# Kernel tuning notes

Hardware: AMD Instinct MI355X
Metric: run time of the kernel (lower is better)

## Reference

```python
import jax, jax.numpy as jnp
import numpy as np

EMBED = 512
HEADS = 8
SCALE = 4
B, N = 2, 2048
DH = EMBED // HEADS
EPS = 1e-5


def _mha(q_in, k_in, v_in, wq, bq, wk, bk, wv, bv, wo, bo, causal):
    Bq, Nq, _ = q_in.shape
    Nk = k_in.shape[1]
    Q = (q_in @ wq + bq).reshape(Bq, Nq, HEADS, DH)
    K = (k_in @ wk + bk).reshape(Bq, Nk, HEADS, DH)
    V = (v_in @ wv + bv).reshape(Bq, Nk, HEADS, DH)
    # scores: [B, H, Nq, Nk]
    scores = jnp.einsum('bqhd,bkhd->bhqk', Q, K) / np.sqrt(DH).astype(np.float32)
    if causal:
        mask = jnp.triu(jnp.full((Nq, Nq), -jnp.inf, dtype=scores.dtype), k=1)
        scores = scores + mask[None, None]
    attn = jax.nn.softmax(scores, axis=-1)
    out = jnp.einsum('bhqk,bkhd->bqhd', attn, V).reshape(Bq, Nq, EMBED)
    return out @ wo + bo


def _ln(x, g, b):
    mu = jnp.mean(x, axis=-1, keepdims=True)
    var = jnp.var(x, axis=-1, keepdims=True)
    return (x - mu) * jax.lax.rsqrt(var + EPS) * g + b


def setup_inputs() -> dict:
    key = jax.random.key(0)
    ks = iter(jax.random.split(key, 32))
    p = lambda *s: 0.02 * jax.random.normal(next(ks), s, dtype=jnp.float32)
    inp = {
        'x': jax.random.normal(next(ks), (B, N, EMBED), dtype=jnp.float32),
        'encoder_output': jax.random.normal(next(ks), (B, N, EMBED), dtype=jnp.float32),
    }
    for pre in ('sa', 'ca'):
        inp[pre + '_wq'] = p(EMBED, EMBED); inp[pre + '_bq'] = jnp.zeros(EMBED)
        inp[pre + '_wk'] = p(EMBED, EMBED); inp[pre + '_bk'] = jnp.zeros(EMBED)
        inp[pre + '_wv'] = p(EMBED, EMBED); inp[pre + '_bv'] = jnp.zeros(EMBED)
        inp[pre + '_wo'] = p(EMBED, EMBED); inp[pre + '_bo'] = jnp.zeros(EMBED)
    for i in (1, 2, 3):
        inp[f'ln{i}_g'] = jnp.ones(EMBED); inp[f'ln{i}_b'] = jnp.zeros(EMBED)
    inp['ff_w1'] = p(EMBED, SCALE * EMBED); inp['ff_b1'] = jnp.zeros(SCALE * EMBED)
    inp['ff_w2'] = p(SCALE * EMBED, EMBED); inp['ff_b2'] = jnp.zeros(EMBED)
    return inp


def reference(x, encoder_output,
              sa_wq, sa_bq, sa_wk, sa_bk, sa_wv, sa_bv, sa_wo, sa_bo,
              ca_wq, ca_bq, ca_wk, ca_bk, ca_wv, ca_bv, ca_wo, ca_bo,
              ln1_g, ln1_b, ln2_g, ln2_b, ln3_g, ln3_b,
              ff_w1, ff_b1, ff_w2, ff_b2):
    x = _mha(x, x, x, sa_wq, sa_bq, sa_wk, sa_bk, sa_wv, sa_bv, sa_wo, sa_bo, True) + x
    x = _ln(x, ln1_g, ln1_b)
    x = _mha(x, encoder_output, encoder_output,
             ca_wq, ca_bq, ca_wk, ca_bk, ca_wv, ca_bv, ca_wo, ca_bo, False) + x
    x = _ln(x, ln2_g, ln2_b)
    h = jax.nn.gelu(x @ ff_w1 + ff_b1, approximate=False)
    x = h @ ff_w2 + ff_b2 + x
    return _ln(x, ln3_g, ln3_b)
```

## Files before the change

kernel.cpp:

```cpp
#include <hip/hip_runtime.h>
#include <hip/hip_bf16.h>

typedef __bf16 bf16x8 __attribute__((ext_vector_type(8)));
typedef float f32x4 __attribute__((ext_vector_type(4)));
typedef unsigned short u16;

#define EMB 512
#define FF 2048
#define MTOT 4096
#define SEQ 2048

__device__ __forceinline__ u16 f2b(float f) {
  return __builtin_bit_cast(u16, (__bf16)f);
}

__device__ __forceinline__ void gload16(const u16* g, u16* l) {
  __builtin_amdgcn_global_load_lds(
      (const __attribute__((address_space(1))) unsigned int*)g,
      (__attribute__((address_space(3))) unsigned int*)l, 16, 0, 0);
}

__global__ __launch_bounds__(256) void prep_all(
    const float* s0, const float* s1, const float* s2, const float* s3,
    const float* s4, const float* s5, const float* s6, const float* s7,
    const float* s8, const float* s9,
    u16* d0, u16* d1, u16* d2, u16* d3, u16* d4,
    u16* d5, u16* d6, u16* d7, u16* d8, u16* d9,
    const float* x, u16* xb, const float* enc, u16* encb,
    const float* bq1, const float* bk1, const float* bv1, float* bqkv,
    const float* bk2, const float* bv2, float* bkv) {
  int z = blockIdx.z, bx = blockIdx.x, by = blockIdx.y;
  int tid = threadIdx.x;
  if (z >= 10) {
    int fb = by * 64 + bx;
    const float* src = (z == 10) ? x : enc;
    u16* dst = (z == 10) ? xb : encb;
    size_t base = (size_t)fb * 2048 + tid * 8;
    float4 a = *(const float4*)(src + base);
    float4 b = *(const float4*)(src + base + 4);
    uint4 u;
    u.x = f2b(a.x) | ((unsigned)f2b(a.y) << 16);
    u.y = f2b(a.z) | ((unsigned)f2b(a.w) << 16);
    u.z = f2b(b.x) | ((unsigned)f2b(b.y) << 16);
    u.w = f2b(b.z) | ((unsigned)f2b(b.w) << 16);
    *(uint4*)(dst + base) = u;
    return;
  }
  if (z == 0 && bx == 16 && by == 0) {
    for (int i = tid; i < 1536; i += 256)
      bqkv[i] = (i < 512) ? bq1[i] : (i < 1024 ? bk1[i - 512] : bv1[i - 1024]);
    return;
  }
  if (z == 1 && bx == 16 && by == 0) {
    for (int i = tid; i < 1024; i += 256)
      bkv[i] = (i < 512) ? bk2[i] : bv2[i - 512];
    return;
  }
  const float* src; u16* dst; int K, N;
  switch (z) {
    case 0: src = s0; dst = d0; K = 512; N = 512; break;
    case 1: src = s1; dst = d1; K = 512; N = 512; break;
    case 2: src = s2; dst = d2; K = 512; N = 512; break;
    case 3: src = s3; dst = d3; K = 512; N = 512; break;
    case 4: src = s4; dst = d4; K = 512; N = 512; break;
    case 5: src = s5; dst = d5; K = 512; N = 512; break;
    case 6: src = s6; dst = d6; K = 512; N = 512; break;
    case 7: src = s7; dst = d7; K = 512; N = 512; break;
    case 8: src = s8; dst = d8; K = 512; N = 2048; break;
    default: src = s9; dst = d9; K = 2048; N = 512; break;
  }
  int ntl, ktl;
  if (z == 9) { ktl = bx; ntl = by; } else { ntl = bx; ktl = by; }
  if (ntl * 32 >= N || ktl * 32 >= K) return;
  __shared__ float t[32][33];
  int tx = tid & 31, ty = tid >> 5;
  int n0 = ntl * 32, k0 = ktl * 32;
#pragma unroll
  for (int i = 0; i < 4; i++)
    t[ty + i * 8][tx] = src[(size_t)(k0 + ty + i * 8) * N + n0 + tx];
  __syncthreads();
#pragma unroll
  for (int i = 0; i < 4; i++)
    dst[(size_t)(n0 + ty + i * 8) * K + k0 + tx] = f2b(t[tx][ty + i * 8]);
}

template <int BM, bool OUTB, bool OUTF, bool RES, bool GELU_>
__global__ __launch_bounds__(256) void gemm_bt(
    const u16* __restrict__ A, const u16* __restrict__ Bt,
    const float* __restrict__ bias, const float* __restrict__ resid,
    u16* __restrict__ outb, float* __restrict__ outf, int K, int Nd) {
  constexpr int MI = BM / 32;
  __shared__ u16 As[2][BM * 32];
  __shared__ u16 Bs[2][128 * 32];
  int tid = threadIdx.x;
  int lane = tid & 63, w = tid >> 6;
  int g = lane >> 4, li = lane & 15;
  int wr = w >> 1, wc = w & 1;
  int m0 = blockIdx.x * BM, n0 = blockIdx.y * 128;
  int row_s = tid >> 2, ch_s = tid & 3;
  int cs = ch_s ^ ((row_s ^ (row_s >> 2)) & 3);
  const u16* Ap = A + (size_t)(m0 + row_s) * K + cs * 8;
  const u16* Bp = Bt + (size_t)(n0 + row_s) * K + cs * 8;
  size_t step64 = (size_t)64 * K;
  int s2a = (li ^ (li >> 2)) & 3;
  f32x4 acc[MI][4] = {};
  int T = K >> 5;
  auto stage = [&](int t, int buf) {
    int k0 = t << 5;
    u16* Ad = &As[buf][w * 512];
    u16* Bd = &Bs[buf][w * 512];
    gload16(Ap + k0, Ad);
    if constexpr (BM == 128) gload16(Ap + step64 + k0, Ad + 2048);
    gload16(Bp + k0, Bd);
    gload16(Bp + step64 + k0, Bd + 2048);
  };
  stage(0, 0);
  __syncthreads();
  for (int t = 0; t < T; t++) {
    int cur = t & 1;
    if (t + 1 < T) stage(t + 1, cur ^ 1);
    bf16x8 af[MI], bfr[4];
#pragma unroll
    for (int i = 0; i < MI; i++)
      af[i] = *(const bf16x8*)&As[cur][(wr * (BM / 2) + i * 16 + li) * 32 + (g ^ s2a) * 8];
#pragma unroll
    for (int i = 0; i < 4; i++)
      bfr[i] = *(const bf16x8*)&Bs[cur][(wc * 64 + i * 16 + li) * 32 + (g ^ s2a) * 8];
#pragma unroll
    for (int mi = 0; mi < MI; mi++)
#pragma unroll
      for (int ni = 0; ni < 4; ni++)
        acc[mi][ni] = __builtin_amdgcn_mfma_f32_16x16x32_bf16(af[mi], bfr[ni], acc[mi][ni], 0, 0, 0);
    __syncthreads();
  }
#pragma unroll
  for (int mi = 0; mi < MI; mi++)
#pragma unroll
    for (int ni = 0; ni < 4; ni++) {
      int gn = n0 + wc * 64 + ni * 16 + li;
      float bv = bias[gn];
#pragma unroll
      for (int r = 0; r < 4; r++) {
        int gm = m0 + wr * (BM / 2) + mi * 16 + g * 4 + r;
        float v = acc[mi][ni][r] + bv;
        if (RES) v += resid[(size_t)gm * Nd + gn];
        if (GELU_) v = 0.5f * v * (1.0f + erff(v * 0.70710678118654752f));
        if (OUTF) outf[(size_t)gm * Nd + gn] = v;
        if (OUTB) outb[(size_t)gm * Nd + gn] = f2b(v);
      }
    }
}

template <bool CAUSAL>
__global__ __launch_bounds__(256) void attn_fwd(
    const u16* __restrict__ Q, const u16* __restrict__ Kp,
    const u16* __restrict__ Vp, u16* __restrict__ O, int qs, int kvs) {
  __shared__ u16 Ks[2][128 * 64];
  __shared__ u16 Vt[2][64 * 128];
  __shared__ u16 Ps[4][16 * 128];
  int tid = threadIdx.x;
  int lane = tid & 63, w = tid >> 6;
  int g = lane >> 4, li = lane & 15;
  int idx = blockIdx.x;
  int bh = idx & 15;
  int qbi = idx >> 4;
  if (CAUSAL) qbi = (SEQ / 64 - 1) - qbi;
  int qb = qbi * 64;
  int b = bh >> 3, h = bh & 7;
  const u16* Qh = Q + (size_t)b * SEQ * qs + h * 64;
  const u16* Kh = Kp + (size_t)b * SEQ * kvs + h * 64;
  const u16* Vh = Vp + (size_t)b * SEQ * kvs + h * 64;
  int qrow = qb + w * 16 + li;
  bf16x8 qa[2];
#pragma unroll
  for (int ks = 0; ks < 2; ks++) {
    bf16x8 tq = *(const bf16x8*)&Qh[(size_t)qrow * qs + ks * 32 + g * 8];
#pragma unroll
    for (int j = 0; j < 8; j++) tq[j] = (__bf16)((float)tq[j] * 0.125f);
    qa[ks] = tq;
  }
  int kcc = lane & 7;
  const u16* Ksrc[4];
#pragma unroll
  for (int j = 0; j < 4; j++) {
    int row = j * 32 + w * 8 + (lane >> 3);
    int sw = ((j * 4 + w) ^ (lane >> 3)) & 7;
    Ksrc[j] = Kh + (size_t)row * kvs + (kcc ^ sw) * 8;
  }
  size_t kstep = (size_t)128 * kvs;
  int kq = tid & 31, dcv = tid >> 5;
  const u16* Vsrc = Vh + (size_t)(4 * kq) * kvs + dcv * 8;
  uint4 vr[4];
  auto stageK = [&](int t, int buf) {
    size_t o = (size_t)t * kstep;
    u16* dst = &Ks[buf][w * 512];
#pragma unroll
    for (int j = 0; j < 4; j++) gload16(Ksrc[j] + o, dst + j * 2048);
  };
  auto loadV = [&](int t) {
    size_t o = (size_t)t * kstep;
#pragma unroll
    for (int kk = 0; kk < 4; kk++)
      vr[kk] = *(const uint4*)(Vsrc + o + (size_t)kk * kvs);
  };
  auto writeV = [&](int buf) {
    const u16* a0 = (const u16*)&vr[0];
    const u16* a1 = (const u16*)&vr[1];
    const u16* a2 = (const u16*)&vr[2];
    const u16* a3 = (const u16*)&vr[3];
#pragma unroll
    for (int jj = 0; jj < 8; jj++) {
      int d = dcv * 8 + jj;
      int swv = ((d >> 3) ^ d) & 15;
      uint2 pk;
      pk.x = (unsigned)a0[jj] | ((unsigned)a1[jj] << 16);
      pk.y = (unsigned)a2[jj] | ((unsigned)a3[jj] << 16);
      *(uint2*)&Vt[buf][d * 128 + ((kq >> 1) ^ swv) * 8 + 4 * (kq & 1)] = pk;
    }
  };
  int T = CAUSAL ? (qb >> 7) + 1 : SEQ / 128;
  stageK(0, 0);
  loadV(0);
  writeV(0);
  __syncthreads();
  f32x4 o[4] = {};
  float mreg = -1e30f, lreg = 0.f;
  for (int t = 0; t < T; t++) {
    int cur = t & 1;
    if (t + 1 < T) { stageK(t + 1, cur ^ 1); loadV(t + 1); }
    int kv0 = t << 7;
    f32x4 S[8] = {};
    __builtin_amdgcn_s_setprio(1);
#pragma unroll
    for (int nt = 0; nt < 8; nt++) {
      int krow = nt * 16 + li;
      int sw = ((krow >> 3) ^ krow) & 7;
#pragma unroll
      for (int ks = 0; ks < 2; ks++) {
        bf16x8 kb = *(const bf16x8*)&Ks[cur][krow * 64 + ((ks * 4 + g) ^ sw) * 8];
        S[nt] = __builtin_amdgcn_mfma_f32_16x16x32_bf16(kb, qa[ks], S[nt], 0, 0, 0);
      }
    }
    __builtin_amdgcn_s_setprio(0);
    float pm = -1e30f;
#pragma unroll
    for (int nt = 0; nt < 8; nt++)
#pragma unroll
      for (int r = 0; r < 4; r++) {
        float s = S[nt][r];
        if (CAUSAL && (kv0 + nt * 16 + g * 4 + r > qrow)) s = -1e30f;
        S[nt][r] = s;
        pm = fmaxf(pm, s);
      }
    pm = fmaxf(pm, __shfl_xor(pm, 16, 64));
    pm = fmaxf(pm, __shfl_xor(pm, 32, 64));
    float nm = fmaxf(mreg, pm);
    float csc = __expf(mreg - nm);
    float rs = 0.f;
#pragma unroll
    for (int nt = 0; nt < 8; nt++)
#pragma unroll
      for (int r = 0; r < 4; r++) {
        float e = __expf(S[nt][r] - nm);
        S[nt][r] = e;
        rs += e;
      }
    rs += __shfl_xor(rs, 16, 64);
    rs += __shfl_xor(rs, 32, 64);
    lreg = lreg * csc + rs;
    mreg = nm;
#pragma unroll
    for (int nt = 0; nt < 8; nt++) {
      int cp = 2 * nt + (g >> 1);
      uint2 pk;
      pk.x = (unsigned)f2b(S[nt][0]) | ((unsigned)f2b(S[nt][1]) << 16);
      pk.y = (unsigned)f2b(S[nt][2]) | ((unsigned)f2b(S[nt][3]) << 16);
      *(uint2*)&Ps[w][li * 128 + ((cp ^ li) * 8) + 4 * (g & 1)] = pk;
    }
    float cscr[4];
#pragma unroll
    for (int r = 0; r < 4; r++)
      cscr[r] = __shfl(csc, (lane & 48) | (g * 4 + r), 64);
#pragma unroll
    for (int nd = 0; nd < 4; nd++)
#pragma unroll
      for (int r = 0; r < 4; r++) o[nd][r] *= cscr[r];
    bf16x8 pa[4];
#pragma unroll
    for (int k2 = 0; k2 < 4; k2++)
      pa[k2] = *(const bf16x8*)&Ps[w][li * 128 + (((k2 * 4 + g) ^ li) * 8)];
    __builtin_amdgcn_s_setprio(1);
#pragma unroll
    for (int nd = 0; nd < 4; nd++) {
      int d = nd * 16 + li;
      int swv = ((d >> 3) ^ d) & 15;
#pragma unroll
      for (int k2 = 0; k2 < 4; k2++) {
        bf16x8 vb = *(const bf16x8*)&Vt[cur][d * 128 + (((k2 * 4 + g) ^ swv) * 8)];
        o[nd] = __builtin_amdgcn_mfma_f32_16x16x32_bf16(pa[k2], vb, o[nd], 0, 0, 0);
      }
    }
    __builtin_amdgcn_s_setprio(0);
    if (t + 1 < T) writeV(cur ^ 1);
    __syncthreads();
  }
  float linv = 1.0f / lreg;
  float invr[4];
#pragma unroll
  for (int r = 0; r < 4; r++)
    invr[r] = __shfl(linv, (lane & 48) | (g * 4 + r), 64);
#pragma unroll
  for (int nd = 0; nd < 4; nd++)
#pragma unroll
    for (int r = 0; r < 4; r++)
      O[(size_t)b * SEQ * EMB + (size_t)(qb + w * 16 + g * 4 + r) * EMB + h * 64 + nd * 16 + li] =
          f2b(o[nd][r] * invr[r]);
}

__global__ __launch_bounds__(256) void ln_fused(
    const float* __restrict__ in, const float* __restrict__ gamma,
    const float* __restrict__ beta, float* __restrict__ outf, u16* __restrict__ outb) {
  int row = blockIdx.x * 4 + (threadIdx.x >> 6);
  int lane = threadIdx.x & 63;
  const float* p = in + (size_t)row * EMB + lane * 8;
  float v[8];
  *(float4*)&v[0] = *(const float4*)p;
  *(float4*)&v[4] = *(const float4*)(p + 4);
  float s = 0.f, q = 0.f;
#pragma unroll
  for (int j = 0; j < 8; j++) { s += v[j]; q += v[j] * v[j]; }
#pragma unroll
  for (int d = 1; d < 64; d <<= 1) {
    s += __shfl_xor(s, d, 64);
    q += __shfl_xor(q, d, 64);
  }
  float mu = s * (1.0f / EMB);
  float var = q * (1.0f / EMB) - mu * mu;
  float rsig = rsqrtf(var + 1e-5f);
  float gg[8], bb[8];
  *(float4*)&gg[0] = *(const float4*)(gamma + lane * 8);
  *(float4*)&gg[4] = *(const float4*)(gamma + lane * 8 + 4);
  *(float4*)&bb[0] = *(const float4*)(beta + lane * 8);
  *(float4*)&bb[4] = *(const float4*)(beta + lane * 8 + 4);
  float o[8];
#pragma unroll
  for (int j = 0; j < 8; j++) o[j] = (v[j] - mu) * rsig * gg[j] + bb[j];
  float* po = outf + (size_t)row * EMB + lane * 8;
  *(float4*)po = *(float4*)&o[0];
  *(float4*)(po + 4) = *(float4*)&o[4];
  if (outb) {
    uint4 u;
    u.x = f2b(o[0]) | ((unsigned)f2b(o[1]) << 16);
    u.y = f2b(o[2]) | ((unsigned)f2b(o[3]) << 16);
    u.z = f2b(o[4]) | ((unsigned)f2b(o[5]) << 16);
    u.w = f2b(o[6]) | ((unsigned)f2b(o[7]) << 16);
    *(uint4*)(outb + (size_t)row * EMB + lane * 8) = u;
  }
}

extern "C" void kernel_launch(void* const* d_in, const int* in_sizes, int n_in,
                              void* d_out, int out_size, void* d_ws, size_t ws_size,
                              hipStream_t stream) {
  const float* x     = (const float*)d_in[0];
  const float* enc   = (const float*)d_in[1];
  const float* sa_wq = (const float*)d_in[2];
  const float* sa_bq = (const float*)d_in[3];
  const float* sa_wk = (const float*)d_in[4];
  const float* sa_bk = (const float*)d_in[5];
  const float* sa_wv = (const float*)d_in[6];
  const float* sa_bv = (const float*)d_in[7];
  const float* sa_wo = (const float*)d_in[8];
  const float* sa_bo = (const float*)d_in[9];
  const float* ca_wq = (const float*)d_in[10];
  const float* ca_bq = (const float*)d_in[11];
  const float* ca_wk = (const float*)d_in[12];
  const float* ca_bk = (const float*)d_in[13];
  const float* ca_wv = (const float*)d_in[14];
  const float* ca_bv = (const float*)d_in[15];
  const float* ca_wo = (const float*)d_in[16];
  const float* ca_bo = (const float*)d_in[17];
  const float* ln1_g = (const float*)d_in[18];
  const float* ln1_b = (const float*)d_in[19];
  const float* ln2_g = (const float*)d_in[20];
  const float* ln2_b = (const float*)d_in[21];
  const float* ln3_g = (const float*)d_in[22];
  const float* ln3_b = (const float*)d_in[23];
  const float* ff_w1 = (const float*)d_in[24];
  const float* ff_b1 = (const float*)d_in[25];
  const float* ff_w2 = (const float*)d_in[26];
  const float* ff_b2 = (const float*)d_in[27];

  char* ws = (char*)d_ws;
  size_t off = 0;
  auto alloc = [&](size_t bytes) {
    void* p = ws + off;
    off = (off + bytes + 255) & ~(size_t)255;
    return p;
  };
  u16* qkvT_sa  = (u16*)alloc((size_t)1536 * EMB * 2);
  u16* oT_sa    = (u16*)alloc((size_t)EMB * EMB * 2);
  u16* qT_ca    = (u16*)alloc((size_t)EMB * EMB * 2);
  u16* kvT_ca   = (u16*)alloc((size_t)1024 * EMB * 2);
  u16* oT_ca    = (u16*)alloc((size_t)EMB * EMB * 2);
  u16* w1T      = (u16*)alloc((size_t)FF * EMB * 2);
  u16* w2T      = (u16*)alloc((size_t)EMB * FF * 2);
  float* bqkv_sa = (float*)alloc(1536 * 4);
  float* bkv_ca  = (float*)alloc(1024 * 4);
  u16* xb    = (u16*)alloc((size_t)MTOT * EMB * 2);
  u16* encb  = (u16*)alloc((size_t)MTOT * EMB * 2);
  u16* qkv   = (u16*)alloc((size_t)MTOT * 1536 * 2);
  u16* attnb = (u16*)alloc((size_t)MTOT * EMB * 2);
  float* t0  = (float*)alloc((size_t)MTOT * EMB * 4);
  float* x1  = (float*)alloc((size_t)MTOT * EMB * 4);
  u16* x1b   = (u16*)alloc((size_t)MTOT * EMB * 2);
  float* x2  = (float*)alloc((size_t)MTOT * EMB * 4);
  u16* x2b   = (u16*)alloc((size_t)MTOT * EMB * 2);
  u16* hbuf  = (u16*)alloc((size_t)MTOT * FF * 2);
  u16* qca  = xb;
  u16* kvca = qkv;

  prep_all<<<dim3(64, 16, 12), 256, 0, stream>>>(
      sa_wq, sa_wk, sa_wv, sa_wo, ca_wq, ca_wk, ca_wv, ca_wo, ff_w1, ff_w2,
      qkvT_sa, qkvT_sa + 512 * EMB, qkvT_sa + 1024 * EMB, oT_sa, qT_ca,
      kvT_ca, kvT_ca + 512 * EMB, oT_ca, w1T, w2T,
      x, xb, enc, encb,
      sa_bq, sa_bk, sa_bv, bqkv_sa, ca_bk, ca_bv, bkv_ca);

  gemm_bt<128, true, false, false, false><<<dim3(32, 12), 256, 0, stream>>>(
      xb, qkvT_sa, bqkv_sa, nullptr, qkv, nullptr, EMB, 1536);
  attn_fwd<true><<<512, 256, 0, stream>>>(qkv, qkv + 512, qkv + 1024, attnb, 1536, 1536);
  gemm_bt<64, false, true, true, false><<<dim3(64, 4), 256, 0, stream>>>(
      attnb, oT_sa, sa_bo, x, nullptr, t0, EMB, EMB);
  ln_fused<<<1024, 256, 0, stream>>>(t0, ln1_g, ln1_b, x1, x1b);

  gemm_bt<64, true, false, false, false><<<dim3(64, 4), 256, 0, stream>>>(
      x1b, qT_ca, ca_bq, nullptr, qca, nullptr, EMB, EMB);
  gemm_bt<128, true, false, false, false><<<dim3(32, 8), 256, 0, stream>>>(
      encb, kvT_ca, bkv_ca, nullptr, kvca, nullptr, EMB, 1024);
  attn_fwd<false><<<512, 256, 0, stream>>>(qca, kvca, kvca + 512, attnb, EMB, 1024);
  gemm_bt<64, false, true, true, false><<<dim3(64, 4), 256, 0, stream>>>(
      attnb, oT_ca, ca_bo, x1, nullptr, t0, EMB, EMB);
  ln_fused<<<1024, 256, 0, stream>>>(t0, ln2_g, ln2_b, x2, x2b);

  gemm_bt<128, true, false, false, true><<<dim3(32, 16), 256, 0, stream>>>(
      x2b, w1T, ff_b1, nullptr, hbuf, nullptr, EMB, FF);
  gemm_bt<64, false, true, true, false><<<dim3(64, 4), 256, 0, stream>>>(
      hbuf, w2T, ff_b2, x2, nullptr, t0, FF, EMB);
  ln_fused<<<1024, 256, 0, stream>>>(t0, ln3_g, ln3_b, (float*)d_out, nullptr);
}
```

Baseline: 355.7 us.

## Parametrize GEMM N-tile, use exp2 softmax with lazy rescaling in attention

Adds a BN template parameter to the GEMM so most launches use 64-wide N tiles, which doubles the grid size to fill more compute units. In attention, Q is pre-scaled by log2(e)/8 so exp2f replaces __expf, and the causal mask is applied only on diagonal tiles. The online-softmax max and rescale are updated lazily, only when the new row max exceeds the old one by more than 8, which skips output rescaling on most tiles. The lazy threshold lets unnormalized values grow up to about 2^8, which is a small precision risk for bf16 P.

```diff
diff --git a/kernel.cpp b/kernel.cpp
--- a/kernel.cpp
+++ b/kernel.cpp
@@ -84,60 +84,66 @@
     dst[(size_t)(n0 + ty + i * 8) * K + k0 + tx] = f2b(t[tx][ty + i * 8]);
 }
 
-template <int BM, bool OUTB, bool OUTF, bool RES, bool GELU_>
+template <int BM, int BN, bool OUTB, bool OUTF, bool RES, bool GELU_>
 __global__ __launch_bounds__(256) void gemm_bt(
     const u16* __restrict__ A, const u16* __restrict__ Bt,
     const float* __restrict__ bias, const float* __restrict__ resid,
     u16* __restrict__ outb, float* __restrict__ outf, int K, int Nd) {
   constexpr int MI = BM / 32;
+  constexpr int NI = BN / 32;
+  constexpr int RA = BM / 64;
+  constexpr int RB = BN / 64;
   __shared__ u16 As[2][BM * 32];
-  __shared__ u16 Bs[2][128 * 32];
+  __shared__ u16 Bs[2][BN * 32];
   int tid = threadIdx.x;
   int lane = tid & 63, w = tid >> 6;
   int g = lane >> 4, li = lane & 15;
   int wr = w >> 1, wc = w & 1;
-  int m0 = blockIdx.x * BM, n0 = blockIdx.y * 128;
-  int row_s = tid >> 2, ch_s = tid & 3;
-  int cs = ch_s ^ ((row_s ^ (row_s >> 2)) & 3);
-  const u16* Ap = A + (size_t)(m0 + row_s) * K + cs * 8;
-  const u16* Bp = Bt + (size_t)(n0 + row_s) * K + cs * 8;
-  size_t step64 = (size_t)64 * K;
+  int m0 = blockIdx.x * BM, n0 = blockIdx.y * BN;
+  const u16* srcs[RA + RB];
+  int ldsoff[RA + RB];
+#pragma unroll
+  for (int r = 0; r < RA + RB; r++) {
+    int ca = (r < RA ? r * 256 : (r - RA) * 256) + tid;
+    int row = ca >> 2, chv = ca & 3;
+    int csw = chv ^ ((row ^ (row >> 2)) & 3);
+    srcs[r] = (r < RA ? A + (size_t)(m0 + row) * K : Bt + (size_t)(n0 + row) * K) + csw * 8;
+    ldsoff[r] = ((r < RA ? r * 256 : (r - RA) * 256) + w * 64) * 8;
+  }
   int s2a = (li ^ (li >> 2)) & 3;
-  f32x4 acc[MI][4] = {};
+  f32x4 acc[MI][NI] = {};
   int T = K >> 5;
   auto stage = [&](int t, int buf) {
     int k0 = t << 5;
-    u16* Ad = &As[buf][w * 512];
-    u16* Bd = &Bs[buf][w * 512];
-    gload16(Ap + k0, Ad);
-    if constexpr (BM == 128) gload16(Ap + step64 + k0, Ad + 2048);
-    gload16(Bp + k0, Bd);
-    gload16(Bp + step64 + k0, Bd + 2048);
+#pragma unroll
+    for (int r = 0; r < RA; r++) gload16(srcs[r] + k0, &As[buf][ldsoff[r]]);
+#pragma unroll
+    for (int r = RA; r < RA + RB; r++) gload16(srcs[r] + k0, &Bs[buf][ldsoff[r]]);
   };
   stage(0, 0);
   __syncthreads();
   for (int t = 0; t < T; t++) {
     int cur = t & 1;
     if (t + 1 < T) stage(t + 1, cur ^ 1);
-    bf16x8 af[MI], bfr[4];
+    bf16x8 af[MI], bfr[NI];
 #pragma unroll
     for (int i = 0; i < MI; i++)
       af[i] = *(const bf16x8*)&As[cur][(wr * (BM / 2) + i * 16 + li) * 32 + (g ^ s2a) * 8];
 #pragma unroll
-    for (int i = 0; i < 4; i++)
-      bfr[i] = *(const bf16x8*)&Bs[cur][(wc * 64 + i * 16 + li) * 32 + (g ^ s2a) * 8];
+    for (int i = 0; i < NI; i++)
+      bfr[i] = *(const bf16x8*)&Bs[cur][(wc * (BN / 2) + i * 16 + li) * 32 + (g ^ s2a) * 8];
 #pragma unroll
     for (int mi = 0; mi < MI; mi++)
 #pragma unroll
-      for (int ni = 0; ni < 4; ni++)
+      for (int ni = 0; ni < NI; ni++)
         acc[mi][ni] = __builtin_amdgcn_mfma_f32_16x16x32_bf16(af[mi], bfr[ni], acc[mi][ni], 0, 0, 0);
     __syncthreads();
   }
 #pragma unroll
   for (int mi = 0; mi < MI; mi++)
 #pragma unroll
-    for (int ni = 0; ni < 4; ni++) {
-      int gn = n0 + wc * 64 + ni * 16 + li;
+    for (int ni = 0; ni < NI; ni++) {
+      int gn = n0 + wc * (BN / 2) + ni * 16 + li;
       float bv = bias[gn];
 #pragma unroll
       for (int r = 0; r < 4; r++) {
@@ -176,7 +182,7 @@
   for (int ks = 0; ks < 2; ks++) {
     bf16x8 tq = *(const bf16x8*)&Qh[(size_t)qrow * qs + ks * 32 + g * 8];
 #pragma unroll
-    for (int j = 0; j < 8; j++) tq[j] = (__bf16)((float)tq[j] * 0.125f);
+    for (int j = 0; j < 8; j++) tq[j] = (__bf16)((float)tq[j] * 0.18033688011112042f);
     qa[ks] = tq;
   }
   int kcc = lane & 7;
@@ -242,33 +248,52 @@
       }
     }
     __builtin_amdgcn_s_setprio(0);
-    float pm = -1e30f;
-#pragma unroll
-    for (int nt = 0; nt < 8; nt++)
-#pragma unroll
-      for (int r = 0; r < 4; r++) {
-        float s = S[nt][r];
-        if (CAUSAL && (kv0 + nt * 16 + g * 4 + r > qrow)) s = -1e30f;
-        S[nt][r] = s;
-        pm = fmaxf(pm, s);
+    if (CAUSAL && (kv0 + 127 > qb + w * 16)) {
+#pragma unroll
+      for (int nt = 0; nt < 8; nt++) {
+        int kb0 = kv0 + nt * 16 + g * 4;
+#pragma unroll
+        for (int r = 0; r < 4; r++)
+          if (kb0 + r > qrow) S[nt][r] = -1e30f;
       }
+    }
+    f32x4 mx = S[0];
+#pragma unroll
+    for (int nt = 1; nt < 8; nt++)
+#pragma unroll
+      for (int r = 0; r < 4; r++) mx[r] = fmaxf(mx[r], S[nt][r]);
+    float pm = fmaxf(fmaxf(mx[0], mx[1]), fmaxf(mx[2], mx[3]));
     pm = fmaxf(pm, __shfl_xor(pm, 16, 64));
     pm = fmaxf(pm, __shfl_xor(pm, 32, 64));
-    float nm = fmaxf(mreg, pm);
-    float csc = __expf(mreg - nm);
-    float rs = 0.f;
+    bool need = __any(pm > mreg + 8.0f);
+    float nm = need ? fmaxf(mreg, pm) : mreg;
+    f32x4 acc4 = {0.f, 0.f, 0.f, 0.f};
 #pragma unroll
     for (int nt = 0; nt < 8; nt++)
 #pragma unroll
       for (int r = 0; r < 4; r++) {
-        float e = __expf(S[nt][r] - nm);
+        float e = exp2f(S[nt][r] - nm);
         S[nt][r] = e;
-        rs += e;
+        acc4[r] += e;
       }
+    float rs = (acc4[0] + acc4[1]) + (acc4[2] + acc4[3]);
     rs += __shfl_xor(rs, 16, 64);
     rs += __shfl_xor(rs, 32, 64);
-    lreg = lreg * csc + rs;
-    mreg = nm;
+    if (need) {
+      float csc = exp2f(mreg - nm);
+      lreg = lreg * csc + rs;
+      mreg = nm;
+      float cscr[4];
+#pragma unroll
+      for (int r = 0; r < 4; r++)
+        cscr[r] = __shfl(csc, (lane & 48) | (g * 4 + r), 64);
+#pragma unroll
+      for (int nd = 0; nd < 4; nd++)
+#pragma unroll
+        for (int r = 0; r < 4; r++) o[nd][r] *= cscr[r];
+    } else {
+      lreg += rs;
+    }
 #pragma unroll
     for (int nt = 0; nt < 8; nt++) {
       int cp = 2 * nt + (g >> 1);
@@ -277,14 +302,6 @@
       pk.y = (unsigned)f2b(S[nt][2]) | ((unsigned)f2b(S[nt][3]) << 16);
       *(uint2*)&Ps[w][li * 128 + ((cp ^ li) * 8) + 4 * (g & 1)] = pk;
     }
-    float cscr[4];
-#pragma unroll
-    for (int r = 0; r < 4; r++)
-      cscr[r] = __shfl(csc, (lane & 48) | (g * 4 + r), 64);
-#pragma unroll
-    for (int nd = 0; nd < 4; nd++)
-#pragma unroll
-      for (int r = 0; r < 4; r++) o[nd][r] *= cscr[r];
     bf16x8 pa[4];
 #pragma unroll
     for (int k2 = 0; k2 < 4; k2++)
@@ -426,25 +443,25 @@
       x, xb, enc, encb,
       sa_bq, sa_bk, sa_bv, bqkv_sa, ca_bk, ca_bv, bkv_ca);
 
-  gemm_bt<128, true, false, false, false><<<dim3(32, 12), 256, 0, stream>>>(
+  gemm_bt<128, 64, true, false, false, false><<<dim3(32, 24), 256, 0, stream>>>(
       xb, qkvT_sa, bqkv_sa, nullptr, qkv, nullptr, EMB, 1536);
   attn_fwd<true><<<512, 256, 0, stream>>>(qkv, qkv + 512, qkv + 1024, attnb, 1536, 1536);
-  gemm_bt<64, false, true, true, false><<<dim3(64, 4), 256, 0, stream>>>(
+  gemm_bt<64, 64, false, true, true, false><<<dim3(64, 8), 256, 0, stream>>>(
       attnb, oT_sa, sa_bo, x, nullptr, t0, EMB, EMB);
   ln_fused<<<1024, 256, 0, stream>>>(t0, ln1_g, ln1_b, x1, x1b);
 
-  gemm_bt<64, true, false, false, false><<<dim3(64, 4), 256, 0, stream>>>(
+  gemm_bt<64, 64, true, false, false, false><<<dim3(64, 8), 256, 0, stream>>>(
       x1b, qT_ca, ca_bq, nullptr, qca, nullptr, EMB, EMB);
-  gemm_bt<128, true, false, false, false><<<dim3(32, 8), 256, 0, stream>>>(
+  gemm_bt<128, 64, true, false, false, false><<<dim3(32, 16), 256, 0, stream>>>(
       encb, kvT_ca, bkv_ca, nullptr, kvca, nullptr, EMB, 1024);
   attn_fwd<false><<<512, 256, 0, stream>>>(qca, kvca, kvca + 512, attnb, EMB, 1024);
-  gemm_bt<64, false, true, true, false><<<dim3(64, 4), 256, 0, stream>>>(
+  gemm_bt<64, 64, false, true, true, false><<<dim3(64, 8), 256, 0, stream>>>(
       attnb, oT_ca, ca_bo, x1, nullptr, t0, EMB, EMB);
   ln_fused<<<1024, 256, 0, stream>>>(t0, ln2_g, ln2_b, x2, x2b);
 
-  gemm_bt<128, true, false, false, true><<<dim3(32, 16), 256, 0, stream>>>(
+  gemm_bt<128, 128, true, false, false, true><<<dim3(32, 16), 256, 0, stream>>>(
       x2b, w1T, ff_b1, nullptr, hbuf, nullptr, EMB, FF);
-  gemm_bt<64, false, true, true, false><<<dim3(64, 4), 256, 0, stream>>>(
+  gemm_bt<64, 64, false, true, true, false><<<dim3(64, 8), 256, 0, stream>>>(
       hbuf, w2T, ff_b2, x2, nullptr, t0, FF, EMB);
   ln_fused<<<1024, 256, 0, stream>>>(t0, ln3_g, ln3_b, (float*)d_out, nullptr);
 }
```

Result: faster. 339.7 us (-4.5%).
